# Kernel optimization log

Measured on AMD Instinct MI355X. Metric: run time of the kernel, lower is better.

Reference implementation:

```python
import jax, jax.numpy as jnp
import numpy as np

B, S, D = 4, 4096, 64

def setup_inputs() -> dict:
    key = jax.random.key(0)
    ks = jax.random.split(key, 6)
    mk = lambda k: jax.random.normal(k, (B, S, D), dtype=jnp.float32)
    return {
        "q_re": mk(ks[0]), "q_im": mk(ks[1]),
        "k_re": mk(ks[2]), "k_im": mk(ks[3]),
        "v_re": mk(ks[4]), "v_im": mk(ks[5]),
    }

def reference(q_re, q_im, k_re, k_im, v_re, v_im):
    # Complex QK^T (no conjugate, matching torch.bmm on complex tensors):
    # (qr + i qi)(kr + i ki)^T -> re = qr kr^T - qi ki^T ; im = qr ki^T + qi kr^T
    d_k = q_re.shape[-1]
    scale = 1.0 / jnp.sqrt(jnp.asarray(d_k, dtype=q_re.dtype))
    s_re = (jnp.einsum('bqd,bkd->bqk', q_re, k_re)
            - jnp.einsum('bqd,bkd->bqk', q_im, k_im)) * scale
    s_im = (jnp.einsum('bqd,bkd->bqk', q_re, k_im)
            + jnp.einsum('bqd,bkd->bqk', q_im, k_re)) * scale
    # softmax over |scores| along key axis; weights are real (imag part is 0)
    w = jax.nn.softmax(jnp.sqrt(s_re * s_re + s_im * s_im), axis=-1)  # [B,S,S]
    # CVDropout is identity in eval mode. Output = real_weights @ complex_values
    o_re = jnp.einsum('bqk,bkd->bqd', w, v_re)
    o_im = jnp.einsum('bqk,bkd->bqd', w, v_im)
    return jnp.stack([o_re, o_im], axis=0)  # [2, B, S, D] (real, imag)
```

## Files before the change

### kernel.cpp

```cpp
#include <hip/hip_runtime.h>
#include <stdint.h>

#define B_    4
#define S_    4096
#define D_    64
#define QBLK  64
#define KVBLK 64
#define NT    (S_ / KVBLK)
#define NELEM (B_ * S_ * D_)
#define BS_   (B_ * S_)

typedef __attribute__((ext_vector_type(8))) short bf16x8;
typedef __attribute__((ext_vector_type(4))) short bf16x4;
typedef __attribute__((ext_vector_type(4))) float f32x4;
typedef __attribute__((ext_vector_type(4))) int   i32x4;
typedef __attribute__((ext_vector_type(4))) unsigned u32x4;
typedef __attribute__((ext_vector_type(4))) _Float16 f16x4;

#define MFMA(a, b, c) __builtin_amdgcn_mfma_f32_16x16x32_bf16(a, b, c, 0, 0, 0)
#define VMWAIT(n) asm volatile("s_waitcnt vmcnt(" #n ")" ::: "memory")
#define BARRIER() do { asm volatile("" ::: "memory"); __builtin_amdgcn_s_barrier(); asm volatile("" ::: "memory"); } while (0)
#define LGKM_FENCE() do { asm volatile("s_waitcnt lgkmcnt(0)" ::: "memory"); __builtin_amdgcn_sched_barrier(0); } while (0)

__device__ __forceinline__ short f2bf(float x) {
    unsigned u = __builtin_bit_cast(unsigned, x);
    u += 0x7FFFu + ((u >> 16) & 1u);
    return (short)(u >> 16);
}

__device__ __forceinline__ unsigned cvtpk(float lo, float hi) {
    unsigned r;
    asm("v_cvt_pk_bf16_f32 %0, %1, %2" : "=v"(r) : "v"(lo), "v"(hi));
    return r;
}

__device__ __forceinline__ void async16(const short* g, short* l) {
    __builtin_amdgcn_global_load_lds(
        (const __attribute__((address_space(1))) unsigned int*)g,
        (__attribute__((address_space(3))) unsigned int*)l, 16, 0, 0);
}

__global__ __launch_bounds__(256)
void prepass_kernel(const float* __restrict__ q_re, const float* __restrict__ q_im,
                    const float* __restrict__ k_re, const float* __restrict__ k_im,
                    const float* __restrict__ v_re, const float* __restrict__ v_im,
                    short* __restrict__ ws) {
    const int bidx = blockIdx.x;
    const int tid  = threadIdx.x;
    if (bidx < 4096) {
        const int idx = bidx * 256 + tid;
        const int tn  = idx >> 18;
        const int e4  = idx & ((1 << 18) - 1);
        const float* s = (tn == 0 ? q_re : tn == 1 ? q_im : tn == 2 ? k_re : k_im)
                         + (size_t)e4 * 4;
        const float sc = (tn < 2) ? 0.125f : 1.0f;
        f32x4 x = *(const f32x4*)s;
        bf16x4 v;
#pragma unroll
        for (int c = 0; c < 4; ++c) v[c] = f2bf(x[c] * sc);
        *(bf16x4*)(ws + (size_t)tn * NELEM + (size_t)e4 * 4) = v;
    } else {
        __shared__ short tile[64][72];
        const int tb   = bidx - 4096;
        const int sb   = tb & 63;
        const int b    = (tb >> 6) & 3;
        const int comp = tb >> 8;
        const float* src = comp ? v_im : v_re;
        short* dst = ws + (size_t)(4 + comp) * NELEM;
#pragma unroll
        for (int i = 0; i < 4; ++i) {
            const int slot = i * 256 + tid;
            const int s  = slot >> 4;
            const int d4 = slot & 15;
            f32x4 x = *(const f32x4*)(src + (((size_t)b * S_) + sb * 64 + s) * D_ + d4 * 4);
#pragma unroll
            for (int c = 0; c < 4; ++c) tile[d4 * 4 + c][s] = f2bf(x[c]);
        }
        __syncthreads();
#pragma unroll
        for (int i = 0; i < 2; ++i) {
            const int slot = i * 256 + tid;
            const int d = slot >> 3;
            const int m = slot & 7;
            const int a = m >> 2, hh = m & 3;
            bf16x8 v;
#pragma unroll
            for (int j = 0; j < 8; ++j)
                v[j] = tile[d][a * 32 + hh * 4 + ((j >> 2) << 4) + (j & 3)];
            *(bf16x8*)(dst + ((size_t)b * 64 + d) * S_ + sb * 64 + m * 8) = v;
        }
    }
}

template<int SPLIT, typename OT>
__global__ __launch_bounds__(256, 4)
void cv_attn_main(const short* __restrict__ wsb,
                  float* __restrict__ out,
                  OT* __restrict__ opart,
                  float* __restrict__ ml)
{
    __shared__ __align__(16) short smem[4 * KVBLK * D_];
    short* kr_s = smem;
    short* ki_s = smem + 4096;
    short* vr_s = smem + 8192;
    short* vi_s = smem + 12288;

    const int tid  = threadIdx.x;
    const int lane = tid & 63;
    const int wv   = tid >> 6;
    const int l15  = lane & 15;
    const int h    = lane >> 4;

    int bid = blockIdx.x;
    const int nwg = B_ * 64 * SPLIT;
    bid = (bid & 7) * (nwg >> 3) + (bid >> 3);
    const int qb = bid & 63;
    const int sp = (bid >> 6) % SPLIT;
    const int b  = bid / (64 * SPLIT);

    const short* qr  = wsb;
    const short* qi  = wsb + (size_t)NELEM;
    const short* kr  = wsb + 2 * (size_t)NELEM;
    const short* ki  = wsb + 3 * (size_t)NELEM;
    const short* vrT = wsb + 4 * (size_t)NELEM;
    const short* viT = wsb + 5 * (size_t)NELEM;

    short* kb0 = smem + l15 * 64 + ((h ^ (l15 & 7)) << 3);
    short* kb1 = smem + l15 * 64 + (((h ^ 4) ^ (l15 & 7)) << 3);

    const int qrow = qb * QBLK + wv * 16 + l15;
    const size_t qoff = ((size_t)b * S_ + qrow) * D_;
    bf16x8 fqr[2], fqi[2], fqn[2];
#pragma unroll
    for (int dh = 0; dh < 2; ++dh) {
        fqr[dh] = *(const bf16x8*)(qr + qoff + dh * 32 + h * 8);
        fqi[dh] = *(const bf16x8*)(qi + qoff + dh * 32 + h * 8);
        i32x4 n = __builtin_bit_cast(i32x4, fqi[dh]) ^ (int)0x80008000;
        fqn[dh] = __builtin_bit_cast(bf16x8, n);
    }

    f32x4 o_re[4], o_im[4];
#pragma unroll
    for (int i = 0; i < 4; ++i) {
        o_re[i] = (f32x4){0.f, 0.f, 0.f, 0.f};
        o_im[i] = (f32x4){0.f, 0.f, 0.f, 0.f};
    }
    float m_run = -1e30f, l_run = 0.f;
    const float L2E = 1.44269504088896f;

    const int r8   = lane >> 3;
    const int u16l = lane & 7;
    constexpr int TPB = NT / SPLIT;

    auto stageK = [&](int t) {
        const int kb = (sp * TPB + t) * KVBLK;
#pragma unroll
        for (int i = 0; i < 2; ++i) {
            const int row   = wv * 16 + i * 8 + r8;
            const int lbase = (wv * 16 + i * 8) * 64;
            const int swz   = (u16l ^ (row & 7)) << 3;
            const size_t koff = ((size_t)b * S_ + kb + row) * 64 + swz;
            async16(kr + koff, kr_s + lbase);
            async16(ki + koff, ki_s + lbase);
        }
    };
    auto stageV = [&](int t) {
        const int kb = (sp * TPB + t) * KVBLK;
#pragma unroll
        for (int i = 0; i < 2; ++i) {
            const int row   = wv * 16 + i * 8 + r8;
            const int lbase = (wv * 16 + i * 8) * 64;
            const int swz   = (u16l ^ (row & 7)) << 3;
            const size_t voff = ((size_t)b * 64 + row) * S_ + kb + swz;
            async16(vrT + voff, vr_s + lbase);
            async16(viT + voff, vi_s + lbase);
        }
    };

    stageK(0);
    stageV(0);

    for (int tt = 0; tt < TPB; ++tt) {
        const bool last = (tt == TPB - 1);

        VMWAIT(4);
        BARRIER();

        f32x4 s_re[4], s_im[4];
#pragma unroll
        for (int c = 0; c < 4; ++c) {
            s_re[c] = (f32x4){0.f, 0.f, 0.f, 0.f};
            s_im[c] = (f32x4){0.f, 0.f, 0.f, 0.f};
        }
        __builtin_amdgcn_s_setprio(1);
#pragma unroll
        for (int c = 0; c < 4; ++c) {
            bf16x8 fkr0 = *(const bf16x8*)(kb0 + c * 1024);
            bf16x8 fkr1 = *(const bf16x8*)(kb1 + c * 1024);
            bf16x8 fki0 = *(const bf16x8*)(kb0 + 4096 + c * 1024);
            bf16x8 fki1 = *(const bf16x8*)(kb1 + 4096 + c * 1024);
            s_re[c] = MFMA(fkr0, fqr[0], s_re[c]);
            s_re[c] = MFMA(fkr1, fqr[1], s_re[c]);
            s_re[c] = MFMA(fki0, fqn[0], s_re[c]);
            s_re[c] = MFMA(fki1, fqn[1], s_re[c]);
            s_im[c] = MFMA(fki0, fqr[0], s_im[c]);
            s_im[c] = MFMA(fki1, fqr[1], s_im[c]);
            s_im[c] = MFMA(fkr0, fqi[0], s_im[c]);
            s_im[c] = MFMA(fkr1, fqi[1], s_im[c]);
        }
        __builtin_amdgcn_s_setprio(0);

        LGKM_FENCE();
        BARRIER();
        if (!last) stageK(tt + 1);

#pragma unroll
        for (int c = 0; c < 4; ++c) {
            f32x4 g = s_re[c] * s_re[c] + s_im[c] * s_im[c];
#pragma unroll
            for (int r = 0; r < 4; ++r) s_re[c][r] = __builtin_amdgcn_sqrtf(g[r]);
        }
        float tmax = s_re[0][0];
#pragma unroll
        for (int c = 0; c < 4; ++c)
#pragma unroll
            for (int r = 0; r < 4; ++r) tmax = fmaxf(tmax, s_re[c][r]);
        tmax = fmaxf(tmax, __shfl_xor(tmax, 16));
        tmax = fmaxf(tmax, __shfl_xor(tmax, 32));

        if (__any(tmax > m_run + 8.0f)) {
            const float m_new = fmaxf(m_run, tmax);
            const float alpha = __builtin_amdgcn_exp2f((m_run - m_new) * L2E);
            l_run *= alpha;
#pragma unroll
            for (int i = 0; i < 4; ++i) { o_re[i] *= alpha; o_im[i] *= alpha; }
            m_run = m_new;
        }
        const float nm = -m_run * L2E;

#pragma unroll
        for (int c = 0; c < 4; ++c)
#pragma unroll
            for (int r = 0; r < 4; ++r)
                s_im[c][r] = __builtin_amdgcn_exp2f(__builtin_fmaf(s_re[c][r], L2E, nm));
        f32x4 ps = s_im[0] + s_im[1] + s_im[2] + s_im[3];
        l_run += (ps[0] + ps[1]) + (ps[2] + ps[3]);

        bf16x8 pb[2];
#pragma unroll
        for (int hf = 0; hf < 2; ++hf) {
            u32x4 w;
            w[0] = cvtpk(s_im[hf * 2][0],     s_im[hf * 2][1]);
            w[1] = cvtpk(s_im[hf * 2][2],     s_im[hf * 2][3]);
            w[2] = cvtpk(s_im[hf * 2 + 1][0], s_im[hf * 2 + 1][1]);
            w[3] = cvtpk(s_im[hf * 2 + 1][2], s_im[hf * 2 + 1][3]);
            pb[hf] = __builtin_bit_cast(bf16x8, w);
        }

        if (!last) { VMWAIT(4); } else { VMWAIT(0); }
        BARRIER();

        __builtin_amdgcn_s_setprio(1);
#pragma unroll
        for (int hf = 0; hf < 2; ++hf) {
            const short* kbh = hf ? kb1 : kb0;
#pragma unroll
            for (int dc = 0; dc < 4; ++dc) {
                bf16x8 av = *(const bf16x8*)(kbh + 8192  + dc * 1024);
                bf16x8 ai = *(const bf16x8*)(kbh + 12288 + dc * 1024);
                o_re[dc] = MFMA(av, pb[hf], o_re[dc]);
                o_im[dc] = MFMA(ai, pb[hf], o_im[dc]);
            }
        }
        __builtin_amdgcn_s_setprio(0);

        LGKM_FENCE();
        BARRIER();
        if (!last) stageV(tt + 1);
    }

    float lt = l_run;
    lt += __shfl_xor(lt, 16);
    lt += __shfl_xor(lt, 32);
    const float inv = (SPLIT == 1) ? (1.0f / lt) : 1.0f;

    float* ol = (float*)smem;

    OT* dst_re;
    OT* dst_im;
    if constexpr (SPLIT == 1) {
        dst_re = (OT*)out + ((size_t)b * S_ + qb * QBLK) * D_;
        dst_im = dst_re + (size_t)NELEM;
    } else {
        const size_t qo = ((size_t)b * S_ + qb * QBLK) * D_;
        dst_re = opart + ((size_t)sp * 2 + 0) * NELEM + qo;
        dst_im = opart + ((size_t)sp * 2 + 1) * NELEM + qo;
    }

    auto store_comp = [&](const f32x4 (&oc)[4], OT* og) {
        __syncthreads();
#pragma unroll
        for (int dc = 0; dc < 4; ++dc)
#pragma unroll
            for (int r = 0; r < 4; ++r)
                ol[(wv * 16 + l15) * 65 + dc * 16 + h * 4 + r] = oc[dc][r] * inv;
        __syncthreads();
#pragma unroll
        for (int i = 0; i < 4; ++i) {
            const int slot = i * 256 + tid;
            const int row  = slot >> 4;
            const int c4   = slot & 15;
            f32x4 v;
#pragma unroll
            for (int j = 0; j < 4; ++j) v[j] = ol[row * 65 + c4 * 4 + j];
            if constexpr (sizeof(OT) == 4) {
                *(f32x4*)((float*)og + (size_t)row * D_ + c4 * 4) = v;
            } else {
                f16x4 hv;
#pragma unroll
                for (int j = 0; j < 4; ++j) hv[j] = (_Float16)v[j];
                *(f16x4*)((_Float16*)og + (size_t)row * D_ + c4 * 4) = hv;
            }
        }
    };
    store_comp(o_re, dst_re);
    store_comp(o_im, dst_im);

    if constexpr (SPLIT > 1) {
        if (lane < 16) {
            const int row = qb * QBLK + wv * 16 + lane;
            const size_t mo = ((size_t)sp * BS_ + (size_t)b * S_ + row) * 2;
            ml[mo]     = m_run;
            ml[mo + 1] = lt;
        }
    }
}

template<int SPLIT, typename OT>
__global__ __launch_bounds__(256)
void cv_attn_combine(const OT* __restrict__ opart, const float* __restrict__ ml,
                     float* __restrict__ out) {
    const int idx  = blockIdx.x * 256 + threadIdx.x;
    const int d4   = idx & 15;
    const int rest = idx >> 4;
    const int row  = rest & (BS_ - 1);
    const int comp = rest >> 14;
    float ms[SPLIT], ls[SPLIT];
    float M = -1e30f;
#pragma unroll
    for (int s = 0; s < SPLIT; ++s) {
        ms[s] = ml[((size_t)s * BS_ + row) * 2];
        ls[s] = ml[((size_t)s * BS_ + row) * 2 + 1];
        M = fmaxf(M, ms[s]);
    }
    float L = 0.f;
    f32x4 acc = (f32x4){0.f, 0.f, 0.f, 0.f};
#pragma unroll
    for (int s = 0; s < SPLIT; ++s) {
        const float w = __builtin_amdgcn_exp2f((ms[s] - M) * 1.44269504088896f);
        L += ls[s] * w;
        const OT* op = opart + ((size_t)(s * 2 + comp)) * NELEM + (size_t)row * D_ + d4 * 4;
        f32x4 o;
        if constexpr (sizeof(OT) == 4) {
            o = *(const f32x4*)op;
        } else {
            f16x4 hv = *(const f16x4*)op;
#pragma unroll
            for (int j = 0; j < 4; ++j) o[j] = (float)hv[j];
        }
        acc += o * w;
    }
    const float invL = 1.0f / L;
    acc *= invL;
    *(f32x4*)(out + (size_t)comp * NELEM + (size_t)row * D_ + d4 * 4) = acc;
}

__global__ __launch_bounds__(256, 1)
void cv_attn_legacy(const float* __restrict__ q_re, const float* __restrict__ q_im,
                    const float* __restrict__ k_re, const float* __restrict__ k_im,
                    const float* __restrict__ v_re, const float* __restrict__ v_im,
                    float* __restrict__ out)
{
    __shared__ __align__(16) short smem[4 * KVBLK * D_];
    short* kr_s = smem;
    short* ki_s = smem + 4096;
    short* vr_s = smem + 8192;
    short* vi_s = smem + 12288;

    const int tid  = threadIdx.x;
    const int lane = tid & 63;
    const int wv   = tid >> 6;
    const int l15  = lane & 15;
    const int h    = lane >> 4;

    const int b  = blockIdx.x >> 6;
    const int qb = blockIdx.x & 63;
    const size_t boff = (size_t)b * S_ * D_;

    const int qrow = qb * QBLK + wv * 16 + l15;
    const float* qrp = q_re + boff + (size_t)qrow * D_;
    const float* qip = q_im + boff + (size_t)qrow * D_;
    bf16x8 fqr[2], fqi[2], fqn[2];
#pragma unroll
    for (int dh = 0; dh < 2; ++dh) {
        const int d0 = dh * 32 + h * 8;
        f32x4 a0 = *(const f32x4*)(qrp + d0);
        f32x4 a1 = *(const f32x4*)(qrp + d0 + 4);
        f32x4 b0 = *(const f32x4*)(qip + d0);
        f32x4 b1 = *(const f32x4*)(qip + d0 + 4);
#pragma unroll
        for (int j = 0; j < 4; ++j) {
            fqr[dh][j] = f2bf(a0[j]); fqr[dh][j + 4] = f2bf(a1[j]);
            fqi[dh][j] = f2bf(b0[j]); fqi[dh][j + 4] = f2bf(b1[j]);
            fqn[dh][j] = f2bf(-b0[j]); fqn[dh][j + 4] = f2bf(-b1[j]);
        }
    }

    f32x4 o_re[4], o_im[4];
#pragma unroll
    for (int i = 0; i < 4; ++i) {
        o_re[i] = (f32x4){0.f, 0.f, 0.f, 0.f};
        o_im[i] = (f32x4){0.f, 0.f, 0.f, 0.f};
    }
    float m_run = -1e30f, l_run = 0.f;
    const float SC = 0.125f * 1.44269504088896f;

    for (int t = 0; t < NT; ++t) {
        const int kb = t * KVBLK;
#pragma unroll
        for (int a = 0; a < 2; ++a) {
            const float* src = (a ? k_im : k_re) + boff;
            short* dst = a ? ki_s : kr_s;
#pragma unroll
            for (int i = 0; i < 2; ++i) {
                const int slot = i * 256 + tid;
                const int row  = slot >> 3;
                const int cb   = slot & 7;
                const float* p = src + (size_t)(kb + row) * D_ + cb * 8;
                f32x4 x0 = *(const f32x4*)p;
                f32x4 x1 = *(const f32x4*)(p + 4);
                bf16x8 v;
#pragma unroll
                for (int j = 0; j < 4; ++j) { v[j] = f2bf(x0[j]); v[j + 4] = f2bf(x1[j]); }
                *(bf16x8*)(dst + row * 64 + ((cb ^ (row & 7)) << 3)) = v;
            }
        }
#pragma unroll
        for (int a = 0; a < 2; ++a) {
            const float* src = (a ? v_im : v_re) + boff;
            short* dst = a ? vi_s : vr_s;
#pragma unroll
            for (int i = 0; i < 4; ++i) {
                const int slot = i * 256 + tid;
                const int k  = slot >> 4;
                const int d4 = slot & 15;
                f32x4 x = *(const f32x4*)(src + (size_t)(kb + k) * D_ + d4 * 4);
#pragma unroll
                for (int c = 0; c < 4; ++c) {
                    const int d = d4 * 4 + c;
                    dst[d * 64 + (((k >> 2) ^ (d & 15)) << 2) + (k & 3)] = f2bf(x[c]);
                }
            }
        }
        __syncthreads();

        f32x4 s_re[4], s_im[4];
#pragma unroll
        for (int c = 0; c < 4; ++c) {
            s_re[c] = (f32x4){0.f, 0.f, 0.f, 0.f};
            s_im[c] = (f32x4){0.f, 0.f, 0.f, 0.f};
        }
#pragma unroll
        for (int c = 0; c < 4; ++c) {
            const int krow = c * 16 + l15;
#pragma unroll
            for (int dh = 0; dh < 2; ++dh) {
                const int u = ((dh * 4 + h) ^ (krow & 7)) << 3;
                bf16x8 fkr = *(const bf16x8*)(kr_s + krow * 64 + u);
                bf16x8 fki = *(const bf16x8*)(ki_s + krow * 64 + u);
                s_re[c] = MFMA(fkr, fqr[dh], s_re[c]);
                s_re[c] = MFMA(fki, fqn[dh], s_re[c]);
                s_im[c] = MFMA(fki, fqr[dh], s_im[c]);
                s_im[c] = MFMA(fkr, fqi[dh], s_im[c]);
            }
        }

        float pv[4][4];
        float tmax = 0.f;
#pragma unroll
        for (int c = 0; c < 4; ++c)
#pragma unroll
            for (int r = 0; r < 4; ++r) {
                const float re = s_re[c][r], im = s_im[c][r];
                const float mg = __builtin_amdgcn_sqrtf(re * re + im * im) * SC;
                pv[c][r] = mg;
                tmax = fmaxf(tmax, mg);
            }
        tmax = fmaxf(tmax, __shfl_xor(tmax, 16));
        tmax = fmaxf(tmax, __shfl_xor(tmax, 32));
        const float m_new = fmaxf(m_run, tmax);
        const float alpha = __builtin_amdgcn_exp2f(m_run - m_new);
        m_run = m_new;
        float psum = 0.f;
#pragma unroll
        for (int c = 0; c < 4; ++c)
#pragma unroll
            for (int r = 0; r < 4; ++r) {
                const float e = __builtin_amdgcn_exp2f(pv[c][r] - m_new);
                pv[c][r] = e;
                psum += e;
            }
        l_run = l_run * alpha + psum;
#pragma unroll
        for (int i = 0; i < 4; ++i) { o_re[i] *= alpha; o_im[i] *= alpha; }

        bf16x8 pb[2];
#pragma unroll
        for (int hf = 0; hf < 2; ++hf)
#pragma unroll
            for (int j = 0; j < 4; ++j) {
                pb[hf][j]     = f2bf(pv[hf * 2][j]);
                pb[hf][j + 4] = f2bf(pv[hf * 2 + 1][j]);
            }

#pragma unroll
        for (int hf = 0; hf < 2; ++hf) {
#pragma unroll
            for (int dc = 0; dc < 4; ++dc) {
                const int d  = dc * 16 + l15;
                const int s0 = (((hf * 8) + h)     ^ l15) << 2;
                const int s1 = (((hf * 8) + 4 + h) ^ l15) << 2;
                bf16x4 r0 = *(const bf16x4*)(vr_s + d * 64 + s0);
                bf16x4 r1 = *(const bf16x4*)(vr_s + d * 64 + s1);
                bf16x4 i0 = *(const bf16x4*)(vi_s + d * 64 + s0);
                bf16x4 i1 = *(const bf16x4*)(vi_s + d * 64 + s1);
                bf16x8 av, ai;
#pragma unroll
                for (int j = 0; j < 4; ++j) {
                    av[j] = r0[j]; av[j + 4] = r1[j];
                    ai[j] = i0[j]; ai[j + 4] = i1[j];
                }
                o_re[dc] = MFMA(av, pb[hf], o_re[dc]);
                o_im[dc] = MFMA(ai, pb[hf], o_im[dc]);
            }
        }
        __syncthreads();
    }

    float lt = l_run;
    lt += __shfl_xor(lt, 16);
    lt += __shfl_xor(lt, 32);
    const float inv = 1.0f / lt;

    float* ol = (float*)smem;
    auto store_comp = [&](const f32x4 (&oc)[4], float* og) {
#pragma unroll
        for (int dc = 0; dc < 4; ++dc)
#pragma unroll
            for (int r = 0; r < 4; ++r)
                ol[(wv * 16 + l15) * 65 + dc * 16 + h * 4 + r] = oc[dc][r] * inv;
        __syncthreads();
#pragma unroll
        for (int i = 0; i < 4; ++i) {
            const int slot = i * 256 + tid;
            const int row  = slot >> 4;
            const int c4   = slot & 15;
            f32x4 v;
#pragma unroll
            for (int j = 0; j < 4; ++j) v[j] = ol[row * 65 + c4 * 4 + j];
            *(f32x4*)(og + (size_t)row * D_ + c4 * 4) = v;
        }
        __syncthreads();
    };

    float* og0 = out + boff + (size_t)(qb * QBLK) * D_;
    store_comp(o_re, og0);
    store_comp(o_im, og0 + (size_t)B_ * S_ * D_);
}

extern "C" void kernel_launch(void* const* d_in, const int* in_sizes, int n_in,
                              void* d_out, int out_size, void* d_ws, size_t ws_size,
                              hipStream_t stream) {
    (void)in_sizes; (void)n_in; (void)out_size;
    const float* q_re = (const float*)d_in[0];
    const float* q_im = (const float*)d_in[1];
    const float* k_re = (const float*)d_in[2];
    const float* k_im = (const float*)d_in[3];
    const float* v_re = (const float*)d_in[4];
    const float* v_im = (const float*)d_in[5];
    float* out = (float*)d_out;

    const size_t bf_bytes = 6 * (size_t)NELEM * 2;
    const size_t need8f32 = bf_bytes + 8 * 2 * (size_t)NELEM * 4 + 8 * (size_t)BS_ * 8;
    const size_t need8f16 = bf_bytes + 8 * 2 * (size_t)NELEM * 2 + 8 * (size_t)BS_ * 8;
    const size_t need4f32 = bf_bytes + 4 * 2 * (size_t)NELEM * 4 + 4 * (size_t)BS_ * 8;

    if (ws_size >= bf_bytes) {
        short* wsb = (short*)d_ws;
        prepass_kernel<<<4608, 256, 0, stream>>>(q_re, q_im, k_re, k_im, v_re, v_im, wsb);
        char* extra = (char*)d_ws + bf_bytes;
        if (ws_size >= need8f32) {
            float* opart = (float*)extra;
            float* ml    = (float*)(extra + 8 * 2 * (size_t)NELEM * 4);
            cv_attn_main<8, float><<<B_ * 64 * 8, 256, 0, stream>>>(wsb, nullptr, opart, ml);
            cv_attn_combine<8, float><<<2048, 256, 0, stream>>>(opart, ml, out);
        } else if (ws_size >= need8f16) {
            _Float16* opart = (_Float16*)extra;
            float* ml = (float*)(extra + 8 * 2 * (size_t)NELEM * 2);
            cv_attn_main<8, _Float16><<<B_ * 64 * 8, 256, 0, stream>>>(wsb, nullptr, opart, ml);
            cv_attn_combine<8, _Float16><<<2048, 256, 0, stream>>>(opart, ml, out);
        } else if (ws_size >= need4f32) {
            float* opart = (float*)extra;
            float* ml    = (float*)(extra + 4 * 2 * (size_t)NELEM * 4);
            cv_attn_main<4, float><<<B_ * 64 * 4, 256, 0, stream>>>(wsb, nullptr, opart, ml);
            cv_attn_combine<4, float><<<2048, 256, 0, stream>>>(opart, ml, out);
        } else {
            cv_attn_main<1, float><<<B_ * 64, 256, 0, stream>>>(wsb, out, out, nullptr);
        }
    } else {
        cv_attn_legacy<<<B_ * 64, 256, 0, stream>>>(q_re, q_im, k_re, k_im, v_re, v_im, out);
    }
}
```

Before: 88.41 us.

## Double-buffer K/V tiles in LDS and switch to split-4 with fp16 partials

Replaces the single LDS buffer, where K and V were staged separately around two barriers per tile, with a ping-pong double buffer. Each tile's K and V are prefetched together into the other buffer, leaving one barrier per iteration. The split-KV factor drops from 8 to 4 and partial outputs are stored as fp16, which roughly halves the partial-output traffic, and the combine now normalises per split. In exchange, LDS use doubles, the occupancy hint falls from 4 to 2 blocks, the grid has fewer blocks, and fp16 partials reduce precision.

```diff
diff --git a/kernel.cpp b/kernel.cpp
--- a/kernel.cpp
+++ b/kernel.cpp
@@ -93,17 +93,13 @@
 }
 
 template<int SPLIT, typename OT>
-__global__ __launch_bounds__(256, 4)
+__global__ __launch_bounds__(256, 2)
 void cv_attn_main(const short* __restrict__ wsb,
                   float* __restrict__ out,
                   OT* __restrict__ opart,
                   float* __restrict__ ml)
 {
-    __shared__ __align__(16) short smem[4 * KVBLK * D_];
-    short* kr_s = smem;
-    short* ki_s = smem + 4096;
-    short* vr_s = smem + 8192;
-    short* vi_s = smem + 12288;
+    __shared__ __align__(16) short smem[2 * 4 * KVBLK * D_];
 
     const int tid  = threadIdx.x;
     const int lane = tid & 63;
@@ -152,7 +148,7 @@
     const int u16l = lane & 7;
     constexpr int TPB = NT / SPLIT;
 
-    auto stageK = [&](int t) {
+    auto stage = [&](int t, int DST) {
         const int kb = (sp * TPB + t) * KVBLK;
 #pragma unroll
         for (int i = 0; i < 2; ++i) {
@@ -160,31 +156,19 @@
             const int lbase = (wv * 16 + i * 8) * 64;
             const int swz   = (u16l ^ (row & 7)) << 3;
             const size_t koff = ((size_t)b * S_ + kb + row) * 64 + swz;
-            async16(kr + koff, kr_s + lbase);
-            async16(ki + koff, ki_s + lbase);
+            async16(kr + koff, smem + DST + lbase);
+            async16(ki + koff, smem + DST + 4096 + lbase);
+            const size_t voff = ((size_t)b * 64 + row) * S_ + kb + swz;
+            async16(vrT + voff, smem + DST + 8192 + lbase);
+            async16(viT + voff, smem + DST + 12288 + lbase);
         }
     };
-    auto stageV = [&](int t) {
-        const int kb = (sp * TPB + t) * KVBLK;
-#pragma unroll
-        for (int i = 0; i < 2; ++i) {
-            const int row   = wv * 16 + i * 8 + r8;
-            const int lbase = (wv * 16 + i * 8) * 64;
-            const int swz   = (u16l ^ (row & 7)) << 3;
-            const size_t voff = ((size_t)b * 64 + row) * S_ + kb + swz;
-            async16(vrT + voff, vr_s + lbase);
-            async16(viT + voff, vi_s + lbase);
-        }
-    };
-
-    stageK(0);
-    stageV(0);
-
-    for (int tt = 0; tt < TPB; ++tt) {
-        const bool last = (tt == TPB - 1);
-
-        VMWAIT(4);
+
+    auto body = [&](int t, int CUR, int OTH) {
+        VMWAIT(0);
+        LGKM_FENCE();
         BARRIER();
+        if (t + 1 < TPB) stage(t + 1, OTH);
 
         f32x4 s_re[4], s_im[4];
 #pragma unroll
@@ -195,10 +179,10 @@
         __builtin_amdgcn_s_setprio(1);
 #pragma unroll
         for (int c = 0; c < 4; ++c) {
-            bf16x8 fkr0 = *(const bf16x8*)(kb0 + c * 1024);
-            bf16x8 fkr1 = *(const bf16x8*)(kb1 + c * 1024);
-            bf16x8 fki0 = *(const bf16x8*)(kb0 + 4096 + c * 1024);
-            bf16x8 fki1 = *(const bf16x8*)(kb1 + 4096 + c * 1024);
+            bf16x8 fkr0 = *(const bf16x8*)(kb0 + CUR + c * 1024);
+            bf16x8 fkr1 = *(const bf16x8*)(kb1 + CUR + c * 1024);
+            bf16x8 fki0 = *(const bf16x8*)(kb0 + CUR + 4096 + c * 1024);
+            bf16x8 fki1 = *(const bf16x8*)(kb1 + CUR + 4096 + c * 1024);
             s_re[c] = MFMA(fkr0, fqr[0], s_re[c]);
             s_re[c] = MFMA(fkr1, fqr[1], s_re[c]);
             s_re[c] = MFMA(fki0, fqn[0], s_re[c]);
@@ -210,10 +194,6 @@
         }
         __builtin_amdgcn_s_setprio(0);
 
-        LGKM_FENCE();
-        BARRIER();
-        if (!last) stageK(tt + 1);
-
 #pragma unroll
         for (int c = 0; c < 4; ++c) {
             f32x4 g = s_re[c] * s_re[c] + s_im[c] * s_im[c];
@@ -257,32 +237,31 @@
             pb[hf] = __builtin_bit_cast(bf16x8, w);
         }
 
-        if (!last) { VMWAIT(4); } else { VMWAIT(0); }
-        BARRIER();
-
         __builtin_amdgcn_s_setprio(1);
 #pragma unroll
         for (int hf = 0; hf < 2; ++hf) {
             const short* kbh = hf ? kb1 : kb0;
 #pragma unroll
             for (int dc = 0; dc < 4; ++dc) {
-                bf16x8 av = *(const bf16x8*)(kbh + 8192  + dc * 1024);
-                bf16x8 ai = *(const bf16x8*)(kbh + 12288 + dc * 1024);
+                bf16x8 av = *(const bf16x8*)(kbh + CUR + 8192  + dc * 1024);
+                bf16x8 ai = *(const bf16x8*)(kbh + CUR + 12288 + dc * 1024);
                 o_re[dc] = MFMA(av, pb[hf], o_re[dc]);
                 o_im[dc] = MFMA(ai, pb[hf], o_im[dc]);
             }
         }
         __builtin_amdgcn_s_setprio(0);
-
-        LGKM_FENCE();
-        BARRIER();
-        if (!last) stageV(tt + 1);
+    };
+
+    stage(0, 0);
+    for (int tt = 0; tt < TPB; tt += 2) {
+        body(tt,     0,     16384);
+        body(tt + 1, 16384, 0);
     }
 
     float lt = l_run;
     lt += __shfl_xor(lt, 16);
     lt += __shfl_xor(lt, 32);
-    const float inv = (SPLIT == 1) ? (1.0f / lt) : 1.0f;
+    const float inv = 1.0f / lt;
 
     float* ol = (float*)smem;
 
@@ -353,12 +332,12 @@
         ls[s] = ml[((size_t)s * BS_ + row) * 2 + 1];
         M = fmaxf(M, ms[s]);
     }
-    float L = 0.f;
+    float W = 0.f;
     f32x4 acc = (f32x4){0.f, 0.f, 0.f, 0.f};
 #pragma unroll
     for (int s = 0; s < SPLIT; ++s) {
-        const float w = __builtin_amdgcn_exp2f((ms[s] - M) * 1.44269504088896f);
-        L += ls[s] * w;
+        const float w = ls[s] * __builtin_amdgcn_exp2f((ms[s] - M) * 1.44269504088896f);
+        W += w;
         const OT* op = opart + ((size_t)(s * 2 + comp)) * NELEM + (size_t)row * D_ + d4 * 4;
         f32x4 o;
         if constexpr (sizeof(OT) == 4) {
@@ -370,8 +349,7 @@
         }
         acc += o * w;
     }
-    const float invL = 1.0f / L;
-    acc *= invL;
+    acc *= (1.0f / W);
     *(f32x4*)(out + (size_t)comp * NELEM + (size_t)row * D_ + d4 * 4) = acc;
 }
 
@@ -591,24 +569,19 @@
     float* out = (float*)d_out;
 
     const size_t bf_bytes = 6 * (size_t)NELEM * 2;
-    const size_t need8f32 = bf_bytes + 8 * 2 * (size_t)NELEM * 4 + 8 * (size_t)BS_ * 8;
-    const size_t need8f16 = bf_bytes + 8 * 2 * (size_t)NELEM * 2 + 8 * (size_t)BS_ * 8;
-    const size_t need4f32 = bf_bytes + 4 * 2 * (size_t)NELEM * 4 + 4 * (size_t)BS_ * 8;
+    const size_t mlsz     = 4 * (size_t)BS_ * 8;
+    const size_t need4f16 = bf_bytes + 4 * 2 * (size_t)NELEM * 2 + mlsz;
+    const size_t need4f32 = bf_bytes + 4 * 2 * (size_t)NELEM * 4 + mlsz;
 
     if (ws_size >= bf_bytes) {
         short* wsb = (short*)d_ws;
         prepass_kernel<<<4608, 256, 0, stream>>>(q_re, q_im, k_re, k_im, v_re, v_im, wsb);
         char* extra = (char*)d_ws + bf_bytes;
-        if (ws_size >= need8f32) {
-            float* opart = (float*)extra;
-            float* ml    = (float*)(extra + 8 * 2 * (size_t)NELEM * 4);
-            cv_attn_main<8, float><<<B_ * 64 * 8, 256, 0, stream>>>(wsb, nullptr, opart, ml);
-            cv_attn_combine<8, float><<<2048, 256, 0, stream>>>(opart, ml, out);
-        } else if (ws_size >= need8f16) {
+        if (ws_size >= need4f16) {
             _Float16* opart = (_Float16*)extra;
-            float* ml = (float*)(extra + 8 * 2 * (size_t)NELEM * 2);
-            cv_attn_main<8, _Float16><<<B_ * 64 * 8, 256, 0, stream>>>(wsb, nullptr, opart, ml);
-            cv_attn_combine<8, _Float16><<<2048, 256, 0, stream>>>(opart, ml, out);
+            float* ml = (float*)(extra + 4 * 2 * (size_t)NELEM * 2);
+            cv_attn_main<4, _Float16><<<B_ * 64 * 4, 256, 0, stream>>>(wsb, nullptr, opart, ml);
+            cv_attn_combine<4, _Float16><<<2048, 256, 0, stream>>>(opart, ml, out);
         } else if (ws_size >= need4f32) {
             float* opart = (float*)extra;
             float* ml    = (float*)(extra + 4 * 2 * (size_t)NELEM * 4);
```

Result: faster. 81.02 us (-8.4%).
